# Performance work log

Hardware: AMD Instinct MI355X
Metric: run time of the kernel (lower is better)

Reference implementation:

```python
import jax, jax.numpy as jnp
import numpy as np

PH = 512          # possible_hidden_units
PA = 512          # possible_activation_functions
NOUT = PH + PA    # n_outputs
H = 24            # n_hidden (hard-coded in module)
L = 32            # layer_limit
B = 8192          # batch_size


def setup_inputs() -> dict:
    key = jax.random.key(0)
    ks = jax.random.split(key, 7)
    k = 1.0 / np.sqrt(H).astype(np.float32)
    uni = lambda kk, sh: jax.random.uniform(kk, sh, jnp.float32, -k, k)
    return {
        "w_ih": uni(ks[0], (4 * H, NOUT)),
        "w_hh": uni(ks[1], (4 * H, H)),
        "b_ih": uni(ks[2], (4 * H,)),
        "b_hh": uni(ks[3], (4 * H,)),
        "w_lin": uni(ks[4], (NOUT, H)),
        "b_lin": uni(ks[5], (NOUT,)),
        # per-step uniforms for categorical inverse-CDF sampling (np.random.rand in torch)
        "u": jax.random.uniform(ks[6], (L, B), jnp.float32),
        "batch_size": B,
        "training": 1,
    }


def reference(w_ih, w_hh, b_ih, b_hh, w_lin, b_lin, u, batch_size, training):
    dtype = w_ih.dtype
    # alternating masks: even step -> hidden-unit actions, odd step -> activation actions
    base = jnp.arange(NOUT)
    mask_even = (base < PH).astype(dtype)
    mask_odd = (base >= PH).astype(dtype)
    parity = (jnp.arange(L) % 2)[:, None]
    masks = jnp.where(parity == 0, mask_even[None, :], mask_odd[None, :])  # [L, NOUT]

    train = bool(training)

    def step(carry, xs):
        h, c, a = carry            # h,c: [B,H]; a: one-hot [B,NOUT]
        mask, u_t = xs             # mask: [NOUT], u_t: [B]
        gates = a @ w_ih.T + b_ih + h @ w_hh.T + b_hh   # [B, 4H]
        ig, fg, gg, og = jnp.split(gates, 4, axis=1)
        i = jax.nn.sigmoid(ig)
        f = jax.nn.sigmoid(fg)
        g = jnp.tanh(gg)
        o = jax.nn.sigmoid(og)
        c = f * c + i * g
        h = o * jnp.tanh(c)
        out = jax.nn.softmax(h @ w_lin.T + b_lin, axis=1) * mask  # [B, NOUT]
        out = out / jnp.sum(out, axis=1, keepdims=True)
        if train:
            action = jnp.argmax(jnp.cumsum(out, axis=1) > u_t[:, None], axis=1)
        else:
            action = jnp.argmax(out, axis=1)
        p = jnp.take_along_axis(out, action[:, None], axis=1)[:, 0]  # [B]
        a_next = jax.nn.one_hot(action, NOUT, dtype=dtype)
        return (h, c, a_next), (p, action)

    init = (
        jnp.zeros((B, H), dtype),
        jnp.zeros((B, H), dtype),
        jnp.zeros((B, NOUT), dtype),
    )
    _, (probs, actions) = jax.lax.scan(step, init, (masks, u))
    # scan stacks along leading (step) axis -> transpose to [B, L]
    return probs.T, actions.T
```

## Files before the change

### kernel.cpp

```cpp
#include <hip/hip_runtime.h>
#include <math.h>

#define NOUTK 1024
#define PHK   512
#define HID   24
#define G4    96
#define LSTEPS 32
#define BATCH 8192
#define EPB   16
#define EPBS  8

struct SmemS {
  float  whhT[HID][G4];
  float  blin[NOUTK];
  float  bihs[G4], bhhs[G4];
  double hsh[EPBS][25];
  double scrM[8][EPBS];
  double scrS[8][EPBS];
  double candr[8][EPBS];
  double tots[8][EPBS];
  double r0sh[EPBS];
  float  ubuf[LSTEPS][EPBS];
  int    candj[8][EPBS];
  int    actsh[EPBS];
};

struct SmemD {
  float  stg[HID][128][8];
  float  whhT[HID][G4];
  float  blin[NOUTK];
  float  bihs[G4], bhhs[G4];
  double hsh[EPB][25];
  double scrM[8][EPB];
  double scrS[8][EPB];
  double candr[8][EPB];
  double tots[8][EPB];
  double r0sh[EPB];
  float  ubuf[LSTEPS][EPB];
  int    candj[8][EPB];
  int    actsh[EPB];
};

__device__ __forceinline__ float bf2f(unsigned short v) {
  union { unsigned u; float f; } x; x.u = ((unsigned)v) << 16; return x.f;
}
__device__ __forceinline__ unsigned short f2bf(float f) {
  unsigned u = __float_as_uint(f);
  unsigned r = 0x7FFFu + ((u >> 16) & 1u);
  return (unsigned short)((u + r) >> 16);
}
__device__ __forceinline__ float bfsnap(float f) { return bf2f(f2bf(f)); }

__global__ void __launch_bounds__(256)
prep_ws(const float* __restrict__ wihf, const float* __restrict__ wlinf,
        float* __restrict__ ws, int total) {
  const int idx = blockIdx.x * 256 + threadIdx.x;
  if (idx >= total) return;
  if (idx < NOUTK * G4) {
    const int j = idx / G4;
    const int r = idx - j * G4;
    ws[idx] = wihf[r * NOUTK + j];
  } else {
    const int i2  = idx - NOUTK * G4;
    const int k   = i2 >> 10;
    const int col = i2 & (NOUTK - 1);
    ws[idx] = wlinf[col * HID + k];
  }
}

__global__ void __launch_bounds__(512, 8)
policy_g(const float* __restrict__ whhf,  const float* __restrict__ bihf,
         const float* __restrict__ bhhf,  const float* __restrict__ blinf,
         const float* __restrict__ uf,    const float* __restrict__ wT,
         const float* __restrict__ wKC,   float* __restrict__ outg) {
  __shared__ SmemS smS;
  SmemS* sm = &smS;
  const int tid  = threadIdx.x;
  const int wave = tid >> 6;
  const int lane = tid & 63;
  const int s    = wave;
  const int le   = lane & 7;
  const int jl   = lane >> 3;
  const int eG   = le;
  const int geL  = blockIdx.x * EPBS + wave;
  const int jgl0 = s * 64 + jl * 8;

  for (int i = tid; i < G4 * HID; i += 512) {
    const int row = i / HID, k = i % HID;
    sm->whhT[k][row] = whhf[i];
  }
  for (int i = tid; i < NOUTK; i += 512) sm->blin[i] = blinf[i];
  if (tid < G4) { sm->bihs[tid] = bihf[tid]; sm->bhhs[tid] = bhhf[tid]; }
  if (tid < EPBS * 25) ((double*)sm->hsh)[tid] = 0.0;
  if (tid < EPBS) sm->actsh[tid] = -1;
  if (tid < LSTEPS * EPBS) {
    const int t = tid >> 3, e = tid & 7;
    sm->ubuf[t][e] = uf[t * BATCH + blockIdx.x * EPBS + e];
  }

  double creg = 0.0;
  __syncthreads();

  for (int t = 0; t < LSTEPS; ++t) {
    const int odd  = t & 1;
    const int base = odd ? PHK : 0;

    if (wave < 4 && (lane & 31) < HID) {
      const int eL = (wave << 1) + (lane >> 5);
      const int rl = lane & 31;
      const int a  = sm->actsh[eL];
      double g0, g1, g2, g3;
#define GATE(Q, GOUT)                                                        \
      { const int row = (Q) * HID + rl;                                      \
        const double colA = (a >= 0) ? (double)wT[a * G4 + row] : 0.0;       \
        double mv = 0.0;                                                     \
        _Pragma("unroll 4")                                                  \
        for (int k = 0; k < HID; ++k)                                        \
          mv = fma(sm->hsh[eL][k], (double)sm->whhT[k][row], mv);            \
        GOUT = ((colA + (double)sm->bihs[row]) + mv) + (double)sm->bhhs[row]; \
        __builtin_amdgcn_sched_barrier(0); }
      GATE(0, g0) GATE(1, g1) GATE(2, g2) GATE(3, g3)
#undef GATE
      const double ig = 1.0 / (1.0 + exp(-g0));
      const double fg = 1.0 / (1.0 + exp(-g1));
      const double gv = tanh(g2);
      const double og = 1.0 / (1.0 + exp(-g3));
      creg = fg * creg + ig * gv;
      sm->hsh[eL][rl] = og * tanh(creg);
    }
    __syncthreads();

    double z0 = 0.0, z1 = 0.0, z2 = 0.0, z3 = 0.0,
           z4 = 0.0, z5 = 0.0, z6 = 0.0, z7 = 0.0;
    const float* __restrict__ wrow = wKC + (base + jgl0);
    #pragma unroll 2
    for (int k = 0; k < HID; ++k) {
      const double hv = sm->hsh[eG][k];
      const float4 wa = *(const float4*)(wrow + k * NOUTK);
      const float4 wb = *(const float4*)(wrow + k * NOUTK + 4);
      z0 = fma(hv, (double)wa.x, z0); z1 = fma(hv, (double)wa.y, z1);
      z2 = fma(hv, (double)wa.z, z2); z3 = fma(hv, (double)wa.w, z3);
      z4 = fma(hv, (double)wb.x, z4); z5 = fma(hv, (double)wb.y, z5);
      z6 = fma(hv, (double)wb.z, z6); z7 = fma(hv, (double)wb.w, z7);
    }
    {
      const float4 ba = *(const float4*)&sm->blin[base + jgl0];
      const float4 bb = *(const float4*)&sm->blin[base + jgl0 + 4];
      z0 += (double)ba.x; z1 += (double)ba.y; z2 += (double)ba.z; z3 += (double)ba.w;
      z4 += (double)bb.x; z5 += (double)bb.y; z6 += (double)bb.z; z7 += (double)bb.w;
    }

    double pm = fmax(fmax(fmax(z0, z1), fmax(z2, z3)),
                     fmax(fmax(z4, z5), fmax(z6, z7)));
    pm = fmax(pm, __shfl_xor(pm, 8));
    pm = fmax(pm, __shfl_xor(pm, 16));
    pm = fmax(pm, __shfl_xor(pm, 32));
    if (jl == 0) sm->scrM[s][eG] = pm;
    __syncthreads();
    double Me;
    {
      const double s0 = sm->scrM[0][eG], s1 = sm->scrM[1][eG],
                   s2 = sm->scrM[2][eG], s3 = sm->scrM[3][eG],
                   s4 = sm->scrM[4][eG], s5 = sm->scrM[5][eG],
                   s6 = sm->scrM[6][eG], s7 = sm->scrM[7][eG];
      Me = fmax(fmax(fmax(s0, s1), fmax(s2, s3)),
                fmax(fmax(s4, s5), fmax(s6, s7)));
    }

    z0 = exp(z0 - Me); z1 = exp(z1 - Me);
    __builtin_amdgcn_sched_barrier(0);
    z2 = exp(z2 - Me); z3 = exp(z3 - Me);
    __builtin_amdgcn_sched_barrier(0);
    z4 = exp(z4 - Me); z5 = exp(z5 - Me);
    __builtin_amdgcn_sched_barrier(0);
    z6 = exp(z6 - Me); z7 = exp(z7 - Me);
    double ps = ((((((z0 + z1) + z2) + z3) + z4) + z5) + z6) + z7;
    ps += __shfl_xor(ps, 8);
    ps += __shfl_xor(ps, 16);
    ps += __shfl_xor(ps, 32);
    if (jl == 0) sm->scrS[s][eG] = ps;
    __syncthreads();
    double inv;
    {
      const double s0 = sm->scrS[0][eG], s1 = sm->scrS[1][eG],
                   s2 = sm->scrS[2][eG], s3 = sm->scrS[3][eG],
                   s4 = sm->scrS[4][eG], s5 = sm->scrS[5][eG],
                   s6 = sm->scrS[6][eG], s7 = sm->scrS[7][eG];
      inv = 1.0 / (((s0 + s1) + (s2 + s3)) + ((s4 + s5) + (s6 + s7)));
    }

    const double p0 = z0 * inv,      p1 = p0 + z1 * inv,
                 p2 = p1 + z2 * inv, p3 = p2 + z3 * inv;
    const double p4 = p3 + z4 * inv, p5 = p4 + z5 * inv,
                 p6 = p5 + z6 * inv, p7 = p6 + z7 * inv;
    double exbase = 0.0, acc = 0.0;
    #pragma unroll
    for (int q2 = 0; q2 < 8; ++q2) {
      const double tq = __shfl(p7, q2 * 8 + le);
      if (q2 == jl) exbase = acc;
      acc += tq;
    }
    if (jl == 0) sm->tots[s][eG] = acc;
    if (s == 0 && lane < 8) sm->r0sh[eG] = p0;
    __syncthreads();

    double sb = exbase;
    for (int i = 0; i < s; ++i) sb += sm->tots[i][eG];
    const double ue = (double)sm->ubuf[t][eG];
    int jloc = 0x7FFFFFFF; double rsel = 0.0;
#define CROSS(R, PR, PRM1)                                                   \
    { const double C = sb + PR;                                              \
      if (jloc == 0x7FFFFFFF && C > ue) {                                    \
        jloc = jgl0 + (R); rsel = ((R) == 0) ? (PR) : ((PR) - (PRM1)); } }
    CROSS(0, p0, p0) CROSS(1, p1, p0) CROSS(2, p2, p1) CROSS(3, p3, p2)
    CROSS(4, p4, p3) CROSS(5, p5, p4) CROSS(6, p6, p5) CROSS(7, p7, p6)
#undef CROSS
    { int oj = __shfl_xor(jloc, 8);  double orr = __shfl_xor(rsel, 8);  if (oj < jloc) { jloc = oj; rsel = orr; } }
    { int oj = __shfl_xor(jloc, 16); double orr = __shfl_xor(rsel, 16); if (oj < jloc) { jloc = oj; rsel = orr; } }
    { int oj = __shfl_xor(jloc, 32); double orr = __shfl_xor(rsel, 32); if (oj < jloc) { jloc = oj; rsel = orr; } }
    if (jl == 0) { sm->candj[s][eG] = jloc; sm->candr[s][eG] = rsel; }
    __syncthreads();

    if (lane < 8) {
      int cj = sm->candj[lane][wave]; double cr = sm->candr[lane][wave];
      { int oj = __shfl_xor(cj, 1); double orr = __shfl_xor(cr, 1); if (oj < cj) { cj = oj; cr = orr; } }
      { int oj = __shfl_xor(cj, 2); double orr = __shfl_xor(cr, 2); if (oj < cj) { cj = oj; cr = orr; } }
      { int oj = __shfl_xor(cj, 4); double orr = __shfl_xor(cr, 4); if (oj < cj) { cj = oj; cr = orr; } }
      if (lane == 0) {
        int actg; double p;
        if (cj == 0x7FFFFFFF) {
          actg = 0;
          p = odd ? 0.0 : sm->r0sh[wave];
        } else {
          actg = base + cj; p = cr;
        }
        sm->actsh[wave] = actg;
        const int io = geL * LSTEPS + t;
        outg[io]                  = bfsnap((float)p);
        outg[BATCH * LSTEPS + io] = bfsnap((float)actg);
      }
    }
    __syncthreads();
  }
}

__global__ void __launch_bounds__(1024)
policy_l(const float* __restrict__ wihf,  const float* __restrict__ whhf,
         const float* __restrict__ bihf,  const float* __restrict__ bhhf,
         const float* __restrict__ wlinf, const float* __restrict__ blinf,
         const float* __restrict__ uf,    const float* __restrict__ wT,
         float* __restrict__ outg) {
  extern __shared__ char smraw[];
  SmemD* sm = (SmemD*)smraw;
  const int tid  = threadIdx.x;
  const int wave = tid >> 6;
  const int lane = tid & 63;
  const int s    = wave & 7;
  const int eg   = (wave >> 3) << 3;
  const int le   = lane & 7;
  const int jl   = lane >> 3;
  const int eG   = eg + le;
  const int geL  = blockIdx.x * EPB + wave;
  const int jgl0 = s * 64 + jl * 8;

  {
    const float4* row4 = (const float4*)(wlinf + tid * HID);
    #pragma unroll
    for (int q = 0; q < 6; ++q) {
      const float4 v = row4[q];
      sm->stg[q * 4 + 0][tid >> 3][tid & 7] = v.x;
      sm->stg[q * 4 + 1][tid >> 3][tid & 7] = v.y;
      sm->stg[q * 4 + 2][tid >> 3][tid & 7] = v.z;
      sm->stg[q * 4 + 3][tid >> 3][tid & 7] = v.w;
    }
  }
  for (int i = tid; i < G4 * HID; i += 1024) {
    const int row = i / HID, k = i % HID;
    sm->whhT[k][row] = whhf[i];
  }
  sm->blin[tid] = blinf[tid];
  if (tid < G4) { sm->bihs[tid] = bihf[tid]; sm->bhhs[tid] = bhhf[tid]; }
  if (tid < EPB * 25) ((double*)sm->hsh)[tid] = 0.0;
  if (tid < EPB) sm->actsh[tid] = -1;
  if (tid < LSTEPS * EPB) {
    const int t = tid >> 4, e = tid & 15;
    sm->ubuf[t][e] = uf[t * BATCH + blockIdx.x * EPB + e];
  }

  double creg = 0.0;
  __syncthreads();

  for (int t = 0; t < LSTEPS; ++t) {
    const int odd  = t & 1;
    const int base = odd ? PHK : 0;
    const int c    = (base >> 3) + s * 8 + jl;

    if (wave < 8 && (lane & 31) < HID) {
      const int eL = (wave << 1) + (lane >> 5);
      const int rl = lane & 31;
      const int a  = sm->actsh[eL];
      double g0, g1, g2, g3;
#define GATE(Q, GOUT)                                                        \
      { const int row = (Q) * HID + rl;                                      \
        const double colA = (a >= 0)                                         \
            ? (double)(wT ? wT[a * G4 + row] : wihf[row * NOUTK + a])        \
            : 0.0;                                                           \
        double mv = 0.0;                                                     \
        _Pragma("unroll 4")                                                  \
        for (int k = 0; k < HID; ++k)                                        \
          mv = fma(sm->hsh[eL][k], (double)sm->whhT[k][row], mv);            \
        GOUT = ((colA + (double)sm->bihs[row]) + mv) + (double)sm->bhhs[row]; \
        __builtin_amdgcn_sched_barrier(0); }
      GATE(0, g0) GATE(1, g1) GATE(2, g2) GATE(3, g3)
#undef GATE
      const double ig = 1.0 / (1.0 + exp(-g0));
      const double fg = 1.0 / (1.0 + exp(-g1));
      const double gv = tanh(g2);
      const double og = 1.0 / (1.0 + exp(-g3));
      creg = fg * creg + ig * gv;
      sm->hsh[eL][rl] = og * tanh(creg);
    }
    __syncthreads();

    double z0 = 0.0, z1 = 0.0, z2 = 0.0, z3 = 0.0,
           z4 = 0.0, z5 = 0.0, z6 = 0.0, z7 = 0.0;
    #pragma unroll 2
    for (int k = 0; k < HID; ++k) {
      const double hv = sm->hsh[eG][k];
      const float4 wa = *(const float4*)&sm->stg[k][c][0];
      const float4 wb = *(const float4*)&sm->stg[k][c][4];
      z0 = fma(hv, (double)wa.x, z0); z1 = fma(hv, (double)wa.y, z1);
      z2 = fma(hv, (double)wa.z, z2); z3 = fma(hv, (double)wa.w, z3);
      z4 = fma(hv, (double)wb.x, z4); z5 = fma(hv, (double)wb.y, z5);
      z6 = fma(hv, (double)wb.z, z6); z7 = fma(hv, (double)wb.w, z7);
    }
    {
      const float4 ba = *(const float4*)&sm->blin[base + jgl0];
      const float4 bb = *(const float4*)&sm->blin[base + jgl0 + 4];
      z0 += (double)ba.x; z1 += (double)ba.y; z2 += (double)ba.z; z3 += (double)ba.w;
      z4 += (double)bb.x; z5 += (double)bb.y; z6 += (double)bb.z; z7 += (double)bb.w;
    }

    double pm = fmax(fmax(fmax(z0, z1), fmax(z2, z3)),
                     fmax(fmax(z4, z5), fmax(z6, z7)));
    pm = fmax(pm, __shfl_xor(pm, 8));
    pm = fmax(pm, __shfl_xor(pm, 16));
    pm = fmax(pm, __shfl_xor(pm, 32));
    if (jl == 0) sm->scrM[s][eG] = pm;
    __syncthreads();
    double Me;
    {
      const double s0 = sm->scrM[0][eG], s1 = sm->scrM[1][eG],
                   s2 = sm->scrM[2][eG], s3 = sm->scrM[3][eG],
                   s4 = sm->scrM[4][eG], s5 = sm->scrM[5][eG],
                   s6 = sm->scrM[6][eG], s7 = sm->scrM[7][eG];
      Me = fmax(fmax(fmax(s0, s1), fmax(s2, s3)),
                fmax(fmax(s4, s5), fmax(s6, s7)));
    }

    z0 = exp(z0 - Me); z1 = exp(z1 - Me);
    __builtin_amdgcn_sched_barrier(0);
    z2 = exp(z2 - Me); z3 = exp(z3 - Me);
    __builtin_amdgcn_sched_barrier(0);
    z4 = exp(z4 - Me); z5 = exp(z5 - Me);
    __builtin_amdgcn_sched_barrier(0);
    z6 = exp(z6 - Me); z7 = exp(z7 - Me);
    double ps = ((((((z0 + z1) + z2) + z3) + z4) + z5) + z6) + z7;
    ps += __shfl_xor(ps, 8);
    ps += __shfl_xor(ps, 16);
    ps += __shfl_xor(ps, 32);
    if (jl == 0) sm->scrS[s][eG] = ps;
    __syncthreads();
    double inv;
    {
      const double s0 = sm->scrS[0][eG], s1 = sm->scrS[1][eG],
                   s2 = sm->scrS[2][eG], s3 = sm->scrS[3][eG],
                   s4 = sm->scrS[4][eG], s5 = sm->scrS[5][eG],
                   s6 = sm->scrS[6][eG], s7 = sm->scrS[7][eG];
      inv = 1.0 / (((s0 + s1) + (s2 + s3)) + ((s4 + s5) + (s6 + s7)));
    }

    const double p0 = z0 * inv,      p1 = p0 + z1 * inv,
                 p2 = p1 + z2 * inv, p3 = p2 + z3 * inv;
    const double p4 = p3 + z4 * inv, p5 = p4 + z5 * inv,
                 p6 = p5 + z6 * inv, p7 = p6 + z7 * inv;
    double exbase = 0.0, acc = 0.0;
    #pragma unroll
    for (int q2 = 0; q2 < 8; ++q2) {
      const double tq = __shfl(p7, q2 * 8 + le);
      if (q2 == jl) exbase = acc;
      acc += tq;
    }
    if (jl == 0) sm->tots[s][eG] = acc;
    if (s == 0 && lane < 8) sm->r0sh[eG] = p0;
    __syncthreads();

    double sb = exbase;
    for (int i = 0; i < s; ++i) sb += sm->tots[i][eG];
    const double ue = (double)sm->ubuf[t][eG];
    int jloc = 0x7FFFFFFF; double rsel = 0.0;
#define CROSS(R, PR, PRM1)                                                   \
    { const double C = sb + PR;                                              \
      if (jloc == 0x7FFFFFFF && C > ue) {                                    \
        jloc = jgl0 + (R); rsel = ((R) == 0) ? (PR) : ((PR) - (PRM1)); } }
    CROSS(0, p0, p0) CROSS(1, p1, p0) CROSS(2, p2, p1) CROSS(3, p3, p2)
    CROSS(4, p4, p3) CROSS(5, p5, p4) CROSS(6, p6, p5) CROSS(7, p7, p6)
#undef CROSS
    { int oj = __shfl_xor(jloc, 8);  double orr = __shfl_xor(rsel, 8);  if (oj < jloc) { jloc = oj; rsel = orr; } }
    { int oj = __shfl_xor(jloc, 16); double orr = __shfl_xor(rsel, 16); if (oj < jloc) { jloc = oj; rsel = orr; } }
    { int oj = __shfl_xor(jloc, 32); double orr = __shfl_xor(rsel, 32); if (oj < jloc) { jloc = oj; rsel = orr; } }
    if (jl == 0) { sm->candj[s][eG] = jloc; sm->candr[s][eG] = rsel; }
    __syncthreads();

    if (lane < 8) {
      int cj = sm->candj[lane][wave]; double cr = sm->candr[lane][wave];
      { int oj = __shfl_xor(cj, 1); double orr = __shfl_xor(cr, 1); if (oj < cj) { cj = oj; cr = orr; } }
      { int oj = __shfl_xor(cj, 2); double orr = __shfl_xor(cr, 2); if (oj < cj) { cj = oj; cr = orr; } }
      { int oj = __shfl_xor(cj, 4); double orr = __shfl_xor(cr, 4); if (oj < cj) { cj = oj; cr = orr; } }
      if (lane == 0) {
        int actg; double p;
        if (cj == 0x7FFFFFFF) {
          actg = 0;
          p = odd ? 0.0 : sm->r0sh[wave];
        } else {
          actg = base + cj; p = cr;
        }
        sm->actsh[wave] = actg;
        const int io = geL * LSTEPS + t;
        outg[io]                  = bfsnap((float)p);
        outg[BATCH * LSTEPS + io] = bfsnap((float)actg);
      }
    }
    __syncthreads();
  }
}

extern "C" void kernel_launch(void* const* d_in, const int* in_sizes, int n_in,
                              void* d_out, int out_size, void* d_ws, size_t ws_size,
                              hipStream_t stream) {
  (void)in_sizes; (void)n_in; (void)out_size;
  constexpr int WIHT_N = NOUTK * G4;
  constexpr int WKC_N  = HID * NOUTK;
  const size_t need_full = (size_t)(WIHT_N + WKC_N) * sizeof(float);
  const size_t need_wt   = (size_t)WIHT_N * sizeof(float);

  if (ws_size >= need_full) {
    const int total = WIHT_N + WKC_N;
    prep_ws<<<(total + 255) / 256, 256, 0, stream>>>(
        (const float*)d_in[0], (const float*)d_in[4], (float*)d_ws, total);
    policy_g<<<BATCH / EPBS, 512, 0, stream>>>(
        (const float*)d_in[1], (const float*)d_in[2], (const float*)d_in[3],
        (const float*)d_in[5], (const float*)d_in[6],
        (const float*)d_ws, (const float*)d_ws + WIHT_N, (float*)d_out);
  } else {
    const float* wT = nullptr;
    if (ws_size >= need_wt) {
      prep_ws<<<(WIHT_N + 255) / 256, 256, 0, stream>>>(
          (const float*)d_in[0], (const float*)d_in[4], (float*)d_ws, WIHT_N);
      wT = (const float*)d_ws;
    }
    hipFuncSetAttribute((const void*)policy_l,
                        hipFuncAttributeMaxDynamicSharedMemorySize,
                        (int)sizeof(SmemD));
    policy_l<<<BATCH / EPB, 1024, sizeof(SmemD), stream>>>(
        (const float*)d_in[0], (const float*)d_in[1], (const float*)d_in[2],
        (const float*)d_in[3], (const float*)d_in[4], (const float*)d_in[5],
        (const float*)d_in[6], wT, (float*)d_out);
  }
}
```

Measured before the change: 826.8 us.

## Drop softmax max pass and defer action reduction into next step's gate phase

Removes the max-reduction stage of the softmax, including its shared scratch and one block barrier, and exponentiates the logits directly. The final cross-wave argmin of sampling candidates and the output writes move into the next timestep's LSTM gate threads, with a tail pass after the loop for the last step. This removes another barrier and the separate reduction phase from each step of the sequential loop. Skipping max subtraction relies on the logits staying small enough for double-precision exp not to overflow.

```diff
diff --git a/kernel.cpp b/kernel.cpp
--- a/kernel.cpp
+++ b/kernel.cpp
@@ -15,14 +15,12 @@
   float  blin[NOUTK];
   float  bihs[G4], bhhs[G4];
   double hsh[EPBS][25];
-  double scrM[8][EPBS];
   double scrS[8][EPBS];
   double candr[8][EPBS];
   double tots[8][EPBS];
   double r0sh[EPBS];
   float  ubuf[LSTEPS][EPBS];
   int    candj[8][EPBS];
-  int    actsh[EPBS];
 };
 
 struct SmemD {
@@ -84,6 +82,7 @@
   const int eG   = le;
   const int geL  = blockIdx.x * EPBS + wave;
   const int jgl0 = s * 64 + jl * 8;
+  (void)geL;
 
   for (int i = tid; i < G4 * HID; i += 512) {
     const int row = i / HID, k = i % HID;
@@ -92,7 +91,6 @@
   for (int i = tid; i < NOUTK; i += 512) sm->blin[i] = blinf[i];
   if (tid < G4) { sm->bihs[tid] = bihf[tid]; sm->bhhs[tid] = bhhf[tid]; }
   if (tid < EPBS * 25) ((double*)sm->hsh)[tid] = 0.0;
-  if (tid < EPBS) sm->actsh[tid] = -1;
   if (tid < LSTEPS * EPBS) {
     const int t = tid >> 3, e = tid & 7;
     sm->ubuf[t][e] = uf[t * BATCH + blockIdx.x * EPBS + e];
@@ -108,7 +106,33 @@
     if (wave < 4 && (lane & 31) < HID) {
       const int eL = (wave << 1) + (lane >> 5);
       const int rl = lane & 31;
-      const int a  = sm->actsh[eL];
+      int a;
+      if (t > 0) {
+        int cj = sm->candj[0][eL]; double cr = sm->candr[0][eL];
+        #pragma unroll 2
+        for (int i = 1; i < 8; ++i) {
+          const int    oj  = sm->candj[i][eL];
+          const double orr = sm->candr[i][eL];
+          if (oj < cj) { cj = oj; cr = orr; }
+        }
+        __builtin_amdgcn_sched_barrier(0);
+        const int pe = (t - 1) & 1;
+        int actg; double p;
+        if (cj == 0x7FFFFFFF) {
+          actg = 0;
+          p = pe ? 0.0 : sm->r0sh[eL];
+        } else {
+          actg = (pe ? PHK : 0) + cj; p = cr;
+        }
+        if (rl == 0) {
+          const int io = (blockIdx.x * EPBS + eL) * LSTEPS + (t - 1);
+          outg[io]                  = bfsnap((float)p);
+          outg[BATCH * LSTEPS + io] = bfsnap((float)actg);
+        }
+        a = actg;
+      } else {
+        a = -1;
+      }
       double g0, g1, g2, g3;
 #define GATE(Q, GOUT)                                                        \
       { const int row = (Q) * HID + rl;                                      \
@@ -150,30 +174,13 @@
       z4 += (double)bb.x; z5 += (double)bb.y; z6 += (double)bb.z; z7 += (double)bb.w;
     }
 
-    double pm = fmax(fmax(fmax(z0, z1), fmax(z2, z3)),
-                     fmax(fmax(z4, z5), fmax(z6, z7)));
-    pm = fmax(pm, __shfl_xor(pm, 8));
-    pm = fmax(pm, __shfl_xor(pm, 16));
-    pm = fmax(pm, __shfl_xor(pm, 32));
-    if (jl == 0) sm->scrM[s][eG] = pm;
-    __syncthreads();
-    double Me;
-    {
-      const double s0 = sm->scrM[0][eG], s1 = sm->scrM[1][eG],
-                   s2 = sm->scrM[2][eG], s3 = sm->scrM[3][eG],
-                   s4 = sm->scrM[4][eG], s5 = sm->scrM[5][eG],
-                   s6 = sm->scrM[6][eG], s7 = sm->scrM[7][eG];
-      Me = fmax(fmax(fmax(s0, s1), fmax(s2, s3)),
-                fmax(fmax(s4, s5), fmax(s6, s7)));
-    }
-
-    z0 = exp(z0 - Me); z1 = exp(z1 - Me);
-    __builtin_amdgcn_sched_barrier(0);
-    z2 = exp(z2 - Me); z3 = exp(z3 - Me);
-    __builtin_amdgcn_sched_barrier(0);
-    z4 = exp(z4 - Me); z5 = exp(z5 - Me);
-    __builtin_amdgcn_sched_barrier(0);
-    z6 = exp(z6 - Me); z7 = exp(z7 - Me);
+    z0 = exp(z0); z1 = exp(z1);
+    __builtin_amdgcn_sched_barrier(0);
+    z2 = exp(z2); z3 = exp(z3);
+    __builtin_amdgcn_sched_barrier(0);
+    z4 = exp(z4); z5 = exp(z5);
+    __builtin_amdgcn_sched_barrier(0);
+    z6 = exp(z6); z7 = exp(z7);
     double ps = ((((((z0 + z1) + z2) + z3) + z4) + z5) + z6) + z7;
     ps += __shfl_xor(ps, 8);
     ps += __shfl_xor(ps, 16);
@@ -220,27 +227,24 @@
     { int oj = __shfl_xor(jloc, 32); double orr = __shfl_xor(rsel, 32); if (oj < jloc) { jloc = oj; rsel = orr; } }
     if (jl == 0) { sm->candj[s][eG] = jloc; sm->candr[s][eG] = rsel; }
     __syncthreads();
-
-    if (lane < 8) {
-      int cj = sm->candj[lane][wave]; double cr = sm->candr[lane][wave];
-      { int oj = __shfl_xor(cj, 1); double orr = __shfl_xor(cr, 1); if (oj < cj) { cj = oj; cr = orr; } }
-      { int oj = __shfl_xor(cj, 2); double orr = __shfl_xor(cr, 2); if (oj < cj) { cj = oj; cr = orr; } }
-      { int oj = __shfl_xor(cj, 4); double orr = __shfl_xor(cr, 4); if (oj < cj) { cj = oj; cr = orr; } }
-      if (lane == 0) {
-        int actg; double p;
-        if (cj == 0x7FFFFFFF) {
-          actg = 0;
-          p = odd ? 0.0 : sm->r0sh[wave];
-        } else {
-          actg = base + cj; p = cr;
-        }
-        sm->actsh[wave] = actg;
-        const int io = geL * LSTEPS + t;
-        outg[io]                  = bfsnap((float)p);
-        outg[BATCH * LSTEPS + io] = bfsnap((float)actg);
-      }
-    }
-    __syncthreads();
+  }
+
+  if (tid < EPBS) {
+    const int e = tid;
+    int cj = sm->candj[0][e]; double cr = sm->candr[0][e];
+    #pragma unroll 2
+    for (int i = 1; i < 8; ++i) {
+      const int    oj  = sm->candj[i][e];
+      const double orr = sm->candr[i][e];
+      if (oj < cj) { cj = oj; cr = orr; }
+    }
+    const int pe = (LSTEPS - 1) & 1;
+    int actg; double p;
+    if (cj == 0x7FFFFFFF) { actg = 0; p = pe ? 0.0 : sm->r0sh[e]; }
+    else                  { actg = (pe ? PHK : 0) + cj; p = cr; }
+    const int io = (blockIdx.x * EPBS + e) * LSTEPS + (LSTEPS - 1);
+    outg[io]                  = bfsnap((float)p);
+    outg[BATCH * LSTEPS + io] = bfsnap((float)actg);
   }
 }
 
```

New measurement: 793.1 us. -4.1%, faster.
